# Kernel tuning notes

Measured on AMD Instinct MI355X. Metric: run time of the kernel, lower is better.

Reference implementation:

```python
import jax, jax.numpy as jnp
import numpy as np

I_SIZE, H_SIZE, O_SIZE = 3, 128, 3
B, T, A = 512, 50, 64


def _xavier(k, shape):
    fan_out, fan_in = shape
    limit = float(np.sqrt(6.0 / (fan_in + fan_out)))
    return jax.random.uniform(k, shape, minval=-limit, maxval=limit, dtype=jnp.float32)


def setup_inputs() -> dict:
    key = jax.random.key(0)
    ks = jax.random.split(key, 6)
    src = jax.random.normal(ks[0], (B, T, A * I_SIZE), dtype=jnp.float32)
    return {
        "src": src,
        "W_ih_enc": _xavier(ks[1], (H_SIZE, I_SIZE)),
        "W_hh_enc": _xavier(ks[2], (H_SIZE, H_SIZE)),
        "b_ih_enc": jnp.zeros((H_SIZE,), jnp.float32),
        "b_hh_enc": jnp.zeros((H_SIZE,), jnp.float32),
        "W_ih_dec": _xavier(ks[3], (H_SIZE, O_SIZE)),
        "W_hh_dec": _xavier(ks[4], (H_SIZE, H_SIZE)),
        "b_ih_dec": jnp.zeros((H_SIZE,), jnp.float32),
        "b_hh_dec": jnp.zeros((H_SIZE,), jnp.float32),
        "fc_W": _xavier(ks[5], (O_SIZE, H_SIZE)),
        "fc_b": jnp.zeros((O_SIZE,), jnp.float32),
        "pred_len": 12,
    }


def reference(src, W_ih_enc, W_hh_enc, b_ih_enc, b_hh_enc,
              W_ih_dec, W_hh_dec, b_ih_dec, b_hh_dec, fc_W, fc_b, pred_len):
    b, t, f = src.shape
    a = f // I_SIZE
    # (b, t, a*I) -> (t, b*a, I): agents batched together (vectorizes the per-agent loop)
    xs = src.reshape(b, t, a, I_SIZE).transpose(1, 0, 2, 3).reshape(t, b * a, I_SIZE)

    def enc_step(h, x_t):
        h = jnp.tanh(x_t @ W_ih_enc.T + b_ih_enc + h @ W_hh_enc.T + b_hh_enc)
        return h, None

    h0 = jnp.zeros((b * a, H_SIZE), src.dtype)
    h_enc, _ = jax.lax.scan(enc_step, h0, xs)

    # decoder input = last observed position of each agent
    dec_in0 = xs[-1]  # (b*a, I)

    def dec_step(carry, _):
        h, inp = carry
        h = jnp.tanh(inp @ W_ih_dec.T + b_ih_dec + h @ W_hh_dec.T + b_hh_dec)
        pred = h @ fc_W.T + fc_b  # (b*a, O)
        return (h, pred), pred

    _, preds = jax.lax.scan(dec_step, (h_enc, dec_in0), None, length=pred_len)
    # (pred_len, b*a, O) -> (b, pred_len, a*O)
    out = preds.reshape(pred_len, b, a, O_SIZE).transpose(1, 0, 2, 3).reshape(b, pred_len, a * O_SIZE)
    return out
```

## Files before the change

### kernel.cpp

```cpp
#include <hip/hip_runtime.h>
#include <stdint.h>

typedef _Float16 f16x8 __attribute__((ext_vector_type(8)));
typedef float f32x4 __attribute__((ext_vector_type(4)));
typedef unsigned int u32x4 __attribute__((ext_vector_type(4)));

#define NT 8
#define NKT 5
#define T_OBS 50
#define PRED 12

#define DEC_OFF 20480
#define FC_OFF  40960
#define WS_ELEMS 43008

__device__ __forceinline__ int unperm(int k) {
  return (k & 3) | (((k >> 3) & 3) << 2) | (((k >> 2) & 1) << 4) | (k & 0x60);
}

__global__ void prep_kernel(const float* __restrict__ Wih_e, const float* __restrict__ Whh_e,
                            const float* __restrict__ bih_e, const float* __restrict__ bhh_e,
                            const float* __restrict__ Wih_d, const float* __restrict__ Whh_d,
                            const float* __restrict__ bih_d, const float* __restrict__ bhh_d,
                            const float* __restrict__ fcW,
                            unsigned short* __restrict__ ws) {
  int idx = blockIdx.x * 256 + threadIdx.x;
  if (idx >= WS_ELEMS) return;
  float val = 0.0f;
  if (idx < FC_OFF) {
    const bool enc = idx < DEC_OFF;
    const int e = enc ? idx : idx - DEC_OFF;
    const int j = e & 7;
    const int lane = (e >> 3) & 63;
    const int rem = e >> 9;
    const int kt = rem % 5;
    const int t = rem / 5;
    const int n = 16 * t + (lane & 15);
    const int kappa = 32 * kt + ((lane >> 4) << 3) + j;
    const float* Wih = enc ? Wih_e : Wih_d;
    const float* Whh = enc ? Whh_e : Whh_d;
    const float* bih = enc ? bih_e : bih_d;
    const float* bhh = enc ? bhh_e : bhh_d;
    if (kappa < 128)       val = Whh[n * 128 + unperm(kappa)];
    else if (kappa < 131)  val = Wih[n * 3 + (kappa - 128)];
    else if (kappa == 131) val = bih[n] + bhh[n];
  } else {
    const int e = idx - FC_OFF;
    const int j = e & 7;
    const int lane = (e >> 3) & 63;
    const int kt = e >> 9;
    const int o = lane & 15;
    const int kappa = 32 * kt + ((lane >> 4) << 3) + j;
    if (o < 3) val = fcW[o * 128 + unperm(kappa)];
  }
  _Float16 h = (_Float16)val;
  ws[idx] = __builtin_bit_cast(unsigned short, h);
}

__device__ __forceinline__ float tanh_fast(float v) {
  float e = __builtin_amdgcn_exp2f(v * 2.8853900817779268f);
  return 1.0f - 2.0f * __builtin_amdgcn_rcpf(1.0f + e);
}

__global__ __launch_bounds__(256, 2) void traj_kernel(
    const float* __restrict__ src, const unsigned short* __restrict__ ws,
    const float* __restrict__ fcb, float* __restrict__ out) {
  const int lane = (int)(threadIdx.x & 63u);
  const int wave = (int)(threadIdx.x >> 6u);
  const int seq = blockIdx.x * 64 + wave * 16 + (lane & 15);
  const int b = seq >> 6;
  const int a = seq & 63;
  const bool act = (lane >> 4) == 0;

  f16x8 A[NT * NKT];
  #pragma unroll
  for (int i = 0; i < NT * NKT; ++i) {
    u32x4 raw = *(const u32x4*)(ws + (size_t)(i * 64 + lane) * 8);
    A[i] = __builtin_bit_cast(f16x8, raw);
  }

  const float* xp = src + (size_t)b * (T_OBS * 192) + a * 3;
  float x0 = xp[0], x1 = xp[1], x2 = xp[2];

  f16x8 Bf[4];
  #pragma unroll
  for (int kt = 0; kt < 4; ++kt) {
    #pragma unroll
    for (int i = 0; i < 8; ++i) Bf[kt][i] = (_Float16)0.0f;
  }
  f16x8 xf;
  #pragma unroll
  for (int i = 0; i < 8; ++i) xf[i] = (_Float16)0.0f;
  if (act) { xf[0] = (_Float16)x0; xf[1] = (_Float16)x1; xf[2] = (_Float16)x2; xf[3] = (_Float16)1.0f; }

  for (int s = 0; s < T_OBS; ++s) {
    const int t2 = (s < T_OBS - 1) ? s + 1 : s;
    const float nx0 = xp[t2 * 192 + 0];
    const float nx1 = xp[t2 * 192 + 1];
    const float nx2 = xp[t2 * 192 + 2];

    f32x4 acc[NT];
    #pragma unroll
    for (int t = 0; t < NT; ++t) acc[t] = (f32x4){0.f, 0.f, 0.f, 0.f};

    #pragma unroll
    for (int kt = 0; kt < 4; ++kt) {
      #pragma unroll
      for (int t = 0; t < NT; ++t)
        acc[t] = __builtin_amdgcn_mfma_f32_16x16x32_f16(A[t * NKT + kt], Bf[kt], acc[t], 0, 0, 0);
    }
    #pragma unroll
    for (int t = 0; t < NT; ++t)
      acc[t] = __builtin_amdgcn_mfma_f32_16x16x32_f16(A[t * NKT + 4], xf, acc[t], 0, 0, 0);

    #pragma unroll
    for (int kt = 0; kt < 4; ++kt) {
      #pragma unroll
      for (int q = 0; q < 4; ++q) {
        Bf[kt][q]     = (_Float16)tanh_fast(acc[2 * kt][q]);
        Bf[kt][4 + q] = (_Float16)tanh_fast(acc[2 * kt + 1][q]);
      }
    }
    x0 = nx0; x1 = nx1; x2 = nx2;
    #pragma unroll
    for (int i = 0; i < 8; ++i) xf[i] = (_Float16)0.0f;
    if (act) { xf[0] = (_Float16)x0; xf[1] = (_Float16)x1; xf[2] = (_Float16)x2; xf[3] = (_Float16)1.0f; }
  }

  #pragma unroll
  for (int i = 0; i < NT * NKT; ++i) {
    u32x4 raw = *(const u32x4*)(ws + DEC_OFF + (size_t)(i * 64 + lane) * 8);
    A[i] = __builtin_bit_cast(f16x8, raw);
  }
  f16x8 Afc[4];
  #pragma unroll
  for (int kt = 0; kt < 4; ++kt) {
    u32x4 raw = *(const u32x4*)(ws + FC_OFF + (size_t)(kt * 64 + lane) * 8);
    Afc[kt] = __builtin_bit_cast(f16x8, raw);
  }
  const float fb0 = fcb[0], fb1 = fcb[1], fb2 = fcb[2];

  float* op = out + (size_t)b * (PRED * 192) + a * 3;

  for (int p = 0; p < PRED; ++p) {
    f32x4 acc[NT];
    #pragma unroll
    for (int t = 0; t < NT; ++t) acc[t] = (f32x4){0.f, 0.f, 0.f, 0.f};

    #pragma unroll
    for (int kt = 0; kt < 4; ++kt) {
      #pragma unroll
      for (int t = 0; t < NT; ++t)
        acc[t] = __builtin_amdgcn_mfma_f32_16x16x32_f16(A[t * NKT + kt], Bf[kt], acc[t], 0, 0, 0);
    }
    #pragma unroll
    for (int t = 0; t < NT; ++t)
      acc[t] = __builtin_amdgcn_mfma_f32_16x16x32_f16(A[t * NKT + 4], xf, acc[t], 0, 0, 0);

    #pragma unroll
    for (int kt = 0; kt < 4; ++kt) {
      #pragma unroll
      for (int q = 0; q < 4; ++q) {
        Bf[kt][q]     = (_Float16)tanh_fast(acc[2 * kt][q]);
        Bf[kt][4 + q] = (_Float16)tanh_fast(acc[2 * kt + 1][q]);
      }
    }

    f32x4 pf = (f32x4){0.f, 0.f, 0.f, 0.f};
    #pragma unroll
    for (int kt = 0; kt < 4; ++kt)
      pf = __builtin_amdgcn_mfma_f32_16x16x32_f16(Afc[kt], Bf[kt], pf, 0, 0, 0);

    const float p0 = pf[0] + fb0;
    const float p1 = pf[1] + fb1;
    const float p2 = pf[2] + fb2;
    if (act) {
      op[p * 192 + 0] = p0;
      op[p * 192 + 1] = p1;
      op[p * 192 + 2] = p2;
    }
    #pragma unroll
    for (int i = 0; i < 8; ++i) xf[i] = (_Float16)0.0f;
    if (act) { xf[0] = (_Float16)p0; xf[1] = (_Float16)p1; xf[2] = (_Float16)p2; xf[3] = (_Float16)1.0f; }
  }
}

extern "C" void kernel_launch(void* const* d_in, const int* in_sizes, int n_in,
                              void* d_out, int out_size, void* d_ws, size_t ws_size,
                              hipStream_t stream) {
  const float* src   = (const float*)d_in[0];
  const float* Wih_e = (const float*)d_in[1];
  const float* Whh_e = (const float*)d_in[2];
  const float* bih_e = (const float*)d_in[3];
  const float* bhh_e = (const float*)d_in[4];
  const float* Wih_d = (const float*)d_in[5];
  const float* Whh_d = (const float*)d_in[6];
  const float* bih_d = (const float*)d_in[7];
  const float* bhh_d = (const float*)d_in[8];
  const float* fcW   = (const float*)d_in[9];
  const float* fcb   = (const float*)d_in[10];
  (void)in_sizes; (void)n_in; (void)out_size; (void)ws_size;

  unsigned short* ws = (unsigned short*)d_ws;

  prep_kernel<<<(WS_ELEMS + 255) / 256, 256, 0, stream>>>(
      Wih_e, Whh_e, bih_e, bhh_e, Wih_d, Whh_d, bih_d, bhh_d, fcW, ws);

  traj_kernel<<<512, 256, 0, stream>>>(src, ws, fcb, (float*)d_out);
}
```

Measured before the change: 98.46 us.

## Split hidden units across four waves with LDS exchange per timestep

Each block now handles 16 sequences, with each of the 4 waves computing 32 of the 128 hidden units. New hidden states are exchanged through a double-buffered shared-memory array with a block barrier each step. The grid grows from 512 to 2048 blocks. This shortens the per-wave dependent MFMA chain and cuts register pressure so more waves can hide latency, at the cost of per-step barriers, LDS traffic, and duplicated fc work.

```diff
diff --git a/kernel.cpp b/kernel.cpp
--- a/kernel.cpp
+++ b/kernel.cpp
@@ -62,21 +62,26 @@
   return 1.0f - 2.0f * __builtin_amdgcn_rcpf(1.0f + e);
 }
 
-__global__ __launch_bounds__(256, 2) void traj_kernel(
+__global__ __launch_bounds__(256, 4) void traj_kernel(
     const float* __restrict__ src, const unsigned short* __restrict__ ws,
     const float* __restrict__ fcb, float* __restrict__ out) {
+  __shared__ unsigned short xch[2][4][64][8];
+
   const int lane = (int)(threadIdx.x & 63u);
-  const int wave = (int)(threadIdx.x >> 6u);
-  const int seq = blockIdx.x * 64 + wave * 16 + (lane & 15);
+  const int w = (int)(threadIdx.x >> 6u);
+  const int seq = blockIdx.x * 16 + (lane & 15);
   const int b = seq >> 6;
   const int a = seq & 63;
   const bool act = (lane >> 4) == 0;
 
-  f16x8 A[NT * NKT];
-  #pragma unroll
-  for (int i = 0; i < NT * NKT; ++i) {
-    u32x4 raw = *(const u32x4*)(ws + (size_t)(i * 64 + lane) * 8);
-    A[i] = __builtin_bit_cast(f16x8, raw);
+  f16x8 A[2 * NKT];
+  #pragma unroll
+  for (int i = 0; i < 2; ++i) {
+    #pragma unroll
+    for (int kt = 0; kt < NKT; ++kt) {
+      u32x4 raw = *(const u32x4*)(ws + (size_t)((((2 * w + i) * NKT) + kt) * 64 + lane) * 8);
+      A[i * NKT + kt] = __builtin_bit_cast(f16x8, raw);
+    }
   }
 
   const float* xp = src + (size_t)b * (T_OBS * 192) + a * 3;
@@ -84,10 +89,10 @@
 
   f16x8 Bf[4];
   #pragma unroll
-  for (int kt = 0; kt < 4; ++kt) {
+  for (int kt = 0; kt < 4; ++kt)
     #pragma unroll
     for (int i = 0; i < 8; ++i) Bf[kt][i] = (_Float16)0.0f;
-  }
+
   f16x8 xf;
   #pragma unroll
   for (int i = 0; i < 8; ++i) xf[i] = (_Float16)0.0f;
@@ -99,28 +104,28 @@
     const float nx1 = xp[t2 * 192 + 1];
     const float nx2 = xp[t2 * 192 + 2];
 
-    f32x4 acc[NT];
-    #pragma unroll
-    for (int t = 0; t < NT; ++t) acc[t] = (f32x4){0.f, 0.f, 0.f, 0.f};
-
+    f32x4 acc0 = (f32x4){0.f, 0.f, 0.f, 0.f};
+    f32x4 acc1 = (f32x4){0.f, 0.f, 0.f, 0.f};
     #pragma unroll
     for (int kt = 0; kt < 4; ++kt) {
-      #pragma unroll
-      for (int t = 0; t < NT; ++t)
-        acc[t] = __builtin_amdgcn_mfma_f32_16x16x32_f16(A[t * NKT + kt], Bf[kt], acc[t], 0, 0, 0);
-    }
-    #pragma unroll
-    for (int t = 0; t < NT; ++t)
-      acc[t] = __builtin_amdgcn_mfma_f32_16x16x32_f16(A[t * NKT + 4], xf, acc[t], 0, 0, 0);
-
-    #pragma unroll
-    for (int kt = 0; kt < 4; ++kt) {
-      #pragma unroll
-      for (int q = 0; q < 4; ++q) {
-        Bf[kt][q]     = (_Float16)tanh_fast(acc[2 * kt][q]);
-        Bf[kt][4 + q] = (_Float16)tanh_fast(acc[2 * kt + 1][q]);
-      }
-    }
+      acc0 = __builtin_amdgcn_mfma_f32_16x16x32_f16(A[kt],       Bf[kt], acc0, 0, 0, 0);
+      acc1 = __builtin_amdgcn_mfma_f32_16x16x32_f16(A[NKT + kt], Bf[kt], acc1, 0, 0, 0);
+    }
+    acc0 = __builtin_amdgcn_mfma_f32_16x16x32_f16(A[4],       xf, acc0, 0, 0, 0);
+    acc1 = __builtin_amdgcn_mfma_f32_16x16x32_f16(A[NKT + 4], xf, acc1, 0, 0, 0);
+
+    f16x8 nb;
+    #pragma unroll
+    for (int q = 0; q < 4; ++q) {
+      nb[q]     = (_Float16)tanh_fast(acc0[q]);
+      nb[4 + q] = (_Float16)tanh_fast(acc1[q]);
+    }
+    *(u32x4*)&xch[s & 1][w][lane][0] = __builtin_bit_cast(u32x4, nb);
+    __syncthreads();
+    #pragma unroll
+    for (int kt = 0; kt < 4; ++kt)
+      Bf[kt] = __builtin_bit_cast(f16x8, *(const u32x4*)&xch[s & 1][kt][lane][0]);
+
     x0 = nx0; x1 = nx1; x2 = nx2;
     #pragma unroll
     for (int i = 0; i < 8; ++i) xf[i] = (_Float16)0.0f;
@@ -128,9 +133,12 @@
   }
 
   #pragma unroll
-  for (int i = 0; i < NT * NKT; ++i) {
-    u32x4 raw = *(const u32x4*)(ws + DEC_OFF + (size_t)(i * 64 + lane) * 8);
-    A[i] = __builtin_bit_cast(f16x8, raw);
+  for (int i = 0; i < 2; ++i) {
+    #pragma unroll
+    for (int kt = 0; kt < NKT; ++kt) {
+      u32x4 raw = *(const u32x4*)(ws + DEC_OFF + (size_t)((((2 * w + i) * NKT) + kt) * 64 + lane) * 8);
+      A[i * NKT + kt] = __builtin_bit_cast(f16x8, raw);
+    }
   }
   f16x8 Afc[4];
   #pragma unroll
@@ -143,28 +151,27 @@
   float* op = out + (size_t)b * (PRED * 192) + a * 3;
 
   for (int p = 0; p < PRED; ++p) {
-    f32x4 acc[NT];
-    #pragma unroll
-    for (int t = 0; t < NT; ++t) acc[t] = (f32x4){0.f, 0.f, 0.f, 0.f};
-
+    f32x4 acc0 = (f32x4){0.f, 0.f, 0.f, 0.f};
+    f32x4 acc1 = (f32x4){0.f, 0.f, 0.f, 0.f};
     #pragma unroll
     for (int kt = 0; kt < 4; ++kt) {
-      #pragma unroll
-      for (int t = 0; t < NT; ++t)
-        acc[t] = __builtin_amdgcn_mfma_f32_16x16x32_f16(A[t * NKT + kt], Bf[kt], acc[t], 0, 0, 0);
-    }
-    #pragma unroll
-    for (int t = 0; t < NT; ++t)
-      acc[t] = __builtin_amdgcn_mfma_f32_16x16x32_f16(A[t * NKT + 4], xf, acc[t], 0, 0, 0);
-
-    #pragma unroll
-    for (int kt = 0; kt < 4; ++kt) {
-      #pragma unroll
-      for (int q = 0; q < 4; ++q) {
-        Bf[kt][q]     = (_Float16)tanh_fast(acc[2 * kt][q]);
-        Bf[kt][4 + q] = (_Float16)tanh_fast(acc[2 * kt + 1][q]);
-      }
-    }
+      acc0 = __builtin_amdgcn_mfma_f32_16x16x32_f16(A[kt],       Bf[kt], acc0, 0, 0, 0);
+      acc1 = __builtin_amdgcn_mfma_f32_16x16x32_f16(A[NKT + kt], Bf[kt], acc1, 0, 0, 0);
+    }
+    acc0 = __builtin_amdgcn_mfma_f32_16x16x32_f16(A[4],       xf, acc0, 0, 0, 0);
+    acc1 = __builtin_amdgcn_mfma_f32_16x16x32_f16(A[NKT + 4], xf, acc1, 0, 0, 0);
+
+    f16x8 nb;
+    #pragma unroll
+    for (int q = 0; q < 4; ++q) {
+      nb[q]     = (_Float16)tanh_fast(acc0[q]);
+      nb[4 + q] = (_Float16)tanh_fast(acc1[q]);
+    }
+    *(u32x4*)&xch[p & 1][w][lane][0] = __builtin_bit_cast(u32x4, nb);
+    __syncthreads();
+    #pragma unroll
+    for (int kt = 0; kt < 4; ++kt)
+      Bf[kt] = __builtin_bit_cast(f16x8, *(const u32x4*)&xch[p & 1][kt][lane][0]);
 
     f32x4 pf = (f32x4){0.f, 0.f, 0.f, 0.f};
     #pragma unroll
@@ -174,7 +181,7 @@
     const float p0 = pf[0] + fb0;
     const float p1 = pf[1] + fb1;
     const float p2 = pf[2] + fb2;
-    if (act) {
+    if (w == 0 && act) {
       op[p * 192 + 0] = p0;
       op[p * 192 + 1] = p1;
       op[p * 192 + 2] = p2;
@@ -206,5 +213,5 @@
   prep_kernel<<<(WS_ELEMS + 255) / 256, 256, 0, stream>>>(
       Wih_e, Whh_e, bih_e, bhh_e, Wih_d, Whh_d, bih_d, bhh_d, fcW, ws);
 
-  traj_kernel<<<512, 256, 0, stream>>>(src, ws, fcb, (float*)d_out);
-}
+  traj_kernel<<<2048, 256, 0, stream>>>(src, ws, fcb, (float*)d_out);
+}
```

Measured after the change: 102.8 us. 4.4% more time.

## Switch RNN to 32x32x16 MFMA with two waves splitting hidden units via LDS

Applied to the files above, without the earlier changes.

The recurrence now uses 32x32x16 MFMAs over 32 sequences per block, replacing 16x16x32 tiles that wasted three quarters of the B columns on inactive lanes. Two waves each compute half of the 128 hidden units and swap their tanh outputs through double-buffered shared memory with a barrier every step. The change also packs f16 conversions with cvt_pkrtz and fuses the tanh tail into an FMA. It adds a per-step __syncthreads and LDS traffic on the serial critical path, and launches twice as many smaller blocks.

```diff
diff --git a/kernel.cpp b/kernel.cpp
--- a/kernel.cpp
+++ b/kernel.cpp
@@ -2,20 +2,19 @@
 #include <stdint.h>
 
 typedef _Float16 f16x8 __attribute__((ext_vector_type(8)));
-typedef float f32x4 __attribute__((ext_vector_type(4)));
+typedef _Float16 f16x2 __attribute__((ext_vector_type(2)));
+typedef float f32x16 __attribute__((ext_vector_type(16)));
 typedef unsigned int u32x4 __attribute__((ext_vector_type(4)));
 
-#define NT 8
-#define NKT 5
 #define T_OBS 50
 #define PRED 12
 
-#define DEC_OFF 20480
-#define FC_OFF  40960
-#define WS_ELEMS 43008
-
-__device__ __forceinline__ int unperm(int k) {
-  return (k & 3) | (((k >> 3) & 3) << 2) | (((k >> 2) & 1) << 4) | (k & 0x60);
+#define DEC_OFF 18432
+#define FC_OFF  36864
+#define WS_ELEMS 40960
+
+__device__ __forceinline__ int swap23(int k) {
+  return (k & ~12) | ((k & 4) << 1) | ((k & 8) >> 1);
 }
 
 __global__ void prep_kernel(const float* __restrict__ Wih_e, const float* __restrict__ Whh_e,
@@ -27,31 +26,34 @@
   int idx = blockIdx.x * 256 + threadIdx.x;
   if (idx >= WS_ELEMS) return;
   float val = 0.0f;
+  const int j = idx & 7;
+  const int lane = (idx >> 3) & 63;
+  const int hi = lane >> 5;
+  const int mlo = lane & 31;
   if (idx < FC_OFF) {
     const bool enc = idx < DEC_OFF;
     const int e = enc ? idx : idx - DEC_OFF;
-    const int j = e & 7;
-    const int lane = (e >> 3) & 63;
     const int rem = e >> 9;
-    const int kt = rem % 5;
-    const int t = rem / 5;
-    const int n = 16 * t + (lane & 15);
-    const int kappa = 32 * kt + ((lane >> 4) << 3) + j;
+    const int kt = rem % 9;
+    const int T = rem / 9;
+    const int m = 32 * T + mlo;
     const float* Wih = enc ? Wih_e : Wih_d;
     const float* Whh = enc ? Whh_e : Whh_d;
     const float* bih = enc ? bih_e : bih_d;
     const float* bhh = enc ? bhh_e : bhh_d;
-    if (kappa < 128)       val = Whh[n * 128 + unperm(kappa)];
-    else if (kappa < 131)  val = Wih[n * 3 + (kappa - 128)];
-    else if (kappa == 131) val = bih[n] + bhh[n];
+    if (kt < 8) {
+      const int kap = 16 * kt + 8 * hi + j;
+      val = Whh[m * 128 + swap23(kap)];
+    } else {
+      const int c = 8 * hi + j;
+      if (c < 3) val = Wih[m * 3 + c];
+      else if (c == 3) val = bih[m] + bhh[m];
+    }
   } else {
     const int e = idx - FC_OFF;
-    const int j = e & 7;
-    const int lane = (e >> 3) & 63;
     const int kt = e >> 9;
-    const int o = lane & 15;
-    const int kappa = 32 * kt + ((lane >> 4) << 3) + j;
-    if (o < 3) val = fcW[o * 128 + unperm(kappa)];
+    const int kap = 16 * kt + 8 * hi + j;
+    if (mlo < 3) val = fcW[mlo * 128 + swap23(kap)];
   }
   _Float16 h = (_Float16)val;
   ws[idx] = __builtin_bit_cast(unsigned short, h);
@@ -59,129 +61,133 @@
 
 __device__ __forceinline__ float tanh_fast(float v) {
   float e = __builtin_amdgcn_exp2f(v * 2.8853900817779268f);
-  return 1.0f - 2.0f * __builtin_amdgcn_rcpf(1.0f + e);
-}
-
-__global__ __launch_bounds__(256, 2) void traj_kernel(
+  return __builtin_fmaf(-2.0f, __builtin_amdgcn_rcpf(1.0f + e), 1.0f);
+}
+
+__device__ __forceinline__ unsigned int pk2(float a, float b) {
+  return __builtin_bit_cast(unsigned int, __builtin_amdgcn_cvt_pkrtz(a, b));
+}
+
+__device__ __forceinline__ f16x8 ldfrag(const unsigned short* p) {
+  return __builtin_bit_cast(f16x8, *(const u32x4*)p);
+}
+
+__global__ __launch_bounds__(128, 2) void traj_kernel(
     const float* __restrict__ src, const unsigned short* __restrict__ ws,
     const float* __restrict__ fcb, float* __restrict__ out) {
+  __shared__ unsigned short xch[2][2][4][64][8];
+
   const int lane = (int)(threadIdx.x & 63u);
-  const int wave = (int)(threadIdx.x >> 6u);
-  const int seq = blockIdx.x * 64 + wave * 16 + (lane & 15);
+  const int w = (int)(threadIdx.x >> 6u);
+  const int seq = blockIdx.x * 32 + (lane & 31);
   const int b = seq >> 6;
   const int a = seq & 63;
-  const bool act = (lane >> 4) == 0;
-
-  f16x8 A[NT * NKT];
-  #pragma unroll
-  for (int i = 0; i < NT * NKT; ++i) {
-    u32x4 raw = *(const u32x4*)(ws + (size_t)(i * 64 + lane) * 8);
-    A[i] = __builtin_bit_cast(f16x8, raw);
-  }
-
-  const float* xp = src + (size_t)b * (T_OBS * 192) + a * 3;
-  float x0 = xp[0], x1 = xp[1], x2 = xp[2];
-
-  f16x8 Bf[4];
-  #pragma unroll
-  for (int kt = 0; kt < 4; ++kt) {
-    #pragma unroll
-    for (int i = 0; i < 8; ++i) Bf[kt][i] = (_Float16)0.0f;
-  }
-  f16x8 xf;
-  #pragma unroll
-  for (int i = 0; i < 8; ++i) xf[i] = (_Float16)0.0f;
-  if (act) { xf[0] = (_Float16)x0; xf[1] = (_Float16)x1; xf[2] = (_Float16)x2; xf[3] = (_Float16)1.0f; }
-
-  for (int s = 0; s < T_OBS; ++s) {
-    const int t2 = (s < T_OBS - 1) ? s + 1 : s;
-    const float nx0 = xp[t2 * 192 + 0];
-    const float nx1 = xp[t2 * 192 + 1];
-    const float nx2 = xp[t2 * 192 + 2];
-
-    f32x4 acc[NT];
-    #pragma unroll
-    for (int t = 0; t < NT; ++t) acc[t] = (f32x4){0.f, 0.f, 0.f, 0.f};
-
-    #pragma unroll
-    for (int kt = 0; kt < 4; ++kt) {
-      #pragma unroll
-      for (int t = 0; t < NT; ++t)
-        acc[t] = __builtin_amdgcn_mfma_f32_16x16x32_f16(A[t * NKT + kt], Bf[kt], acc[t], 0, 0, 0);
-    }
-    #pragma unroll
-    for (int t = 0; t < NT; ++t)
-      acc[t] = __builtin_amdgcn_mfma_f32_16x16x32_f16(A[t * NKT + 4], xf, acc[t], 0, 0, 0);
-
-    #pragma unroll
-    for (int kt = 0; kt < 4; ++kt) {
-      #pragma unroll
-      for (int q = 0; q < 4; ++q) {
-        Bf[kt][q]     = (_Float16)tanh_fast(acc[2 * kt][q]);
-        Bf[kt][4 + q] = (_Float16)tanh_fast(acc[2 * kt + 1][q]);
-      }
-    }
-    x0 = nx0; x1 = nx1; x2 = nx2;
-    #pragma unroll
-    for (int i = 0; i < 8; ++i) xf[i] = (_Float16)0.0f;
-    if (act) { xf[0] = (_Float16)x0; xf[1] = (_Float16)x1; xf[2] = (_Float16)x2; xf[3] = (_Float16)1.0f; }
-  }
-
-  #pragma unroll
-  for (int i = 0; i < NT * NKT; ++i) {
-    u32x4 raw = *(const u32x4*)(ws + DEC_OFF + (size_t)(i * 64 + lane) * 8);
-    A[i] = __builtin_bit_cast(f16x8, raw);
-  }
-  f16x8 Afc[4];
-  #pragma unroll
-  for (int kt = 0; kt < 4; ++kt) {
-    u32x4 raw = *(const u32x4*)(ws + FC_OFF + (size_t)(kt * 64 + lane) * 8);
-    Afc[kt] = __builtin_bit_cast(f16x8, raw);
-  }
+
+  f16x8 A[2][9];
+  #pragma unroll
+  for (int t = 0; t < 2; ++t)
+    #pragma unroll
+    for (int kt = 0; kt < 9; ++kt)
+      A[t][kt] = ldfrag(ws + (size_t)(((2 * w + t) * 9 + kt) * 64 + lane) * 8);
+
+  const float* xq = src + (size_t)b * (T_OBS * 192) + a * 3;
+  float x0 = xq[0], x1 = xq[1], x2 = xq[2];
+  xq += 192;
+
+  f16x8 Bf[8];
+  #pragma unroll
+  for (int kt = 0; kt < 8; ++kt) {
+    u32x4 zz = (u32x4)0u;
+    Bf[kt] = __builtin_bit_cast(f16x8, zz);
+  }
+
+  u32x4 xfu = (u32x4)0u;
+  xfu[0] = pk2(x0, x1);
+  xfu[1] = pk2(x2, 1.0f);
+
+  const f32x16 z = (f32x16)0.0f;
+
+  auto rnn_step = [&](int par) {
+    f16x8 xf = __builtin_bit_cast(f16x8, xfu);
+    f32x16 a0 = __builtin_amdgcn_mfma_f32_32x32x16_f16(A[0][8], xf, z, 0, 0, 0);
+    f32x16 a1 = __builtin_amdgcn_mfma_f32_32x32x16_f16(A[1][8], xf, z, 0, 0, 0);
+    #pragma unroll
+    for (int kt = 0; kt < 8; ++kt) {
+      a0 = __builtin_amdgcn_mfma_f32_32x32x16_f16(A[0][kt], Bf[kt], a0, 0, 0, 0);
+      a1 = __builtin_amdgcn_mfma_f32_32x32x16_f16(A[1][kt], Bf[kt], a1, 0, 0, 0);
+    }
+    u32x4 F0, F1, F2, F3;
+    #pragma unroll
+    for (int q = 0; q < 4; ++q) {
+      F0[q] = pk2(tanh_fast(a0[2 * q]),     tanh_fast(a0[2 * q + 1]));
+      F1[q] = pk2(tanh_fast(a0[8 + 2 * q]), tanh_fast(a0[8 + 2 * q + 1]));
+      F2[q] = pk2(tanh_fast(a1[2 * q]),     tanh_fast(a1[2 * q + 1]));
+      F3[q] = pk2(tanh_fast(a1[8 + 2 * q]), tanh_fast(a1[8 + 2 * q + 1]));
+    }
+    *(u32x4*)&xch[par][w][0][lane][0] = F0;
+    *(u32x4*)&xch[par][w][1][lane][0] = F1;
+    *(u32x4*)&xch[par][w][2][lane][0] = F2;
+    *(u32x4*)&xch[par][w][3][lane][0] = F3;
+    __syncthreads();
+    if (w == 0) {
+      Bf[0] = __builtin_bit_cast(f16x8, F0);
+      Bf[1] = __builtin_bit_cast(f16x8, F1);
+      Bf[2] = __builtin_bit_cast(f16x8, F2);
+      Bf[3] = __builtin_bit_cast(f16x8, F3);
+      Bf[4] = ldfrag(&xch[par][1][0][lane][0]);
+      Bf[5] = ldfrag(&xch[par][1][1][lane][0]);
+      Bf[6] = ldfrag(&xch[par][1][2][lane][0]);
+      Bf[7] = ldfrag(&xch[par][1][3][lane][0]);
+    } else {
+      Bf[4] = __builtin_bit_cast(f16x8, F0);
+      Bf[5] = __builtin_bit_cast(f16x8, F1);
+      Bf[6] = __builtin_bit_cast(f16x8, F2);
+      Bf[7] = __builtin_bit_cast(f16x8, F3);
+      Bf[0] = ldfrag(&xch[par][0][0][lane][0]);
+      Bf[1] = ldfrag(&xch[par][0][1][lane][0]);
+      Bf[2] = ldfrag(&xch[par][0][2][lane][0]);
+      Bf[3] = ldfrag(&xch[par][0][3][lane][0]);
+    }
+  };
+
+  for (int s = 0; s < T_OBS - 1; ++s) {
+    const float nx0 = xq[0], nx1 = xq[1], nx2 = xq[2];
+    xq += 192;
+    rnn_step(s & 1);
+    xfu[0] = pk2(nx0, nx1);
+    xfu[1] = pk2(nx2, 1.0f);
+  }
+  rnn_step(1);
+
+  #pragma unroll
+  for (int t = 0; t < 2; ++t)
+    #pragma unroll
+    for (int kt = 0; kt < 9; ++kt)
+      A[t][kt] = ldfrag(ws + DEC_OFF + (size_t)(((2 * w + t) * 9 + kt) * 64 + lane) * 8);
+  f16x8 Afc[8];
+  #pragma unroll
+  for (int kt = 0; kt < 8; ++kt)
+    Afc[kt] = ldfrag(ws + FC_OFF + (size_t)(kt * 64 + lane) * 8);
   const float fb0 = fcb[0], fb1 = fcb[1], fb2 = fcb[2];
 
   float* op = out + (size_t)b * (PRED * 192) + a * 3;
 
   for (int p = 0; p < PRED; ++p) {
-    f32x4 acc[NT];
-    #pragma unroll
-    for (int t = 0; t < NT; ++t) acc[t] = (f32x4){0.f, 0.f, 0.f, 0.f};
-
-    #pragma unroll
-    for (int kt = 0; kt < 4; ++kt) {
-      #pragma unroll
-      for (int t = 0; t < NT; ++t)
-        acc[t] = __builtin_amdgcn_mfma_f32_16x16x32_f16(A[t * NKT + kt], Bf[kt], acc[t], 0, 0, 0);
-    }
-    #pragma unroll
-    for (int t = 0; t < NT; ++t)
-      acc[t] = __builtin_amdgcn_mfma_f32_16x16x32_f16(A[t * NKT + 4], xf, acc[t], 0, 0, 0);
-
-    #pragma unroll
-    for (int kt = 0; kt < 4; ++kt) {
-      #pragma unroll
-      for (int q = 0; q < 4; ++q) {
-        Bf[kt][q]     = (_Float16)tanh_fast(acc[2 * kt][q]);
-        Bf[kt][4 + q] = (_Float16)tanh_fast(acc[2 * kt + 1][q]);
-      }
-    }
-
-    f32x4 pf = (f32x4){0.f, 0.f, 0.f, 0.f};
-    #pragma unroll
-    for (int kt = 0; kt < 4; ++kt)
-      pf = __builtin_amdgcn_mfma_f32_16x16x32_f16(Afc[kt], Bf[kt], pf, 0, 0, 0);
-
+    rnn_step(p & 1);
+    f32x16 pf = __builtin_amdgcn_mfma_f32_32x32x16_f16(Afc[0], Bf[0], z, 0, 0, 0);
+    #pragma unroll
+    for (int kt = 1; kt < 8; ++kt)
+      pf = __builtin_amdgcn_mfma_f32_32x32x16_f16(Afc[kt], Bf[kt], pf, 0, 0, 0);
     const float p0 = pf[0] + fb0;
     const float p1 = pf[1] + fb1;
     const float p2 = pf[2] + fb2;
-    if (act) {
+    if (w == 0 && lane < 32) {
       op[p * 192 + 0] = p0;
       op[p * 192 + 1] = p1;
       op[p * 192 + 2] = p2;
     }
-    #pragma unroll
-    for (int i = 0; i < 8; ++i) xf[i] = (_Float16)0.0f;
-    if (act) { xf[0] = (_Float16)p0; xf[1] = (_Float16)p1; xf[2] = (_Float16)p2; xf[3] = (_Float16)1.0f; }
+    xfu[0] = pk2(p0, p1);
+    xfu[1] = pk2(p2, 1.0f);
   }
 }
 
@@ -206,5 +212,5 @@
   prep_kernel<<<(WS_ELEMS + 255) / 256, 256, 0, stream>>>(
       Wih_e, Whh_e, bih_e, bhh_e, Wih_d, Whh_d, bih_d, bhh_d, fcW, ws);
 
-  traj_kernel<<<512, 256, 0, stream>>>(src, ws, fcb, (float*)d_out);
-}
+  traj_kernel<<<1024, 128, 0, stream>>>(src, ws, fcb, (float*)d_out);
+}
```

Measured after the change: 205.8 us. 109% more time.

## Split hidden dimension across waves with LDS exchange of recurrent state

Applied to the files above, without the earlier changes.

Each block now handles 32 sequences, and each of its four waves computes a 32-row slice of the hidden state for two 16-sequence groups, instead of one wave computing all 128 rows for 16 sequences. The new hidden-state slices are exchanged through double-buffered shared memory with a block barrier every step. The k-tile order is rotated per wave so the locally produced fragment is reused directly. The goal is to cut the serial MFMA chain per wave, lower register pressure (launch bounds go to 3 blocks per SIMD) and double the grid, at the cost of a __syncthreads and LDS traffic on every recurrent step. Packed fp16 conversion via cvt_pkrtz is also used.

```diff
diff --git a/kernel.cpp b/kernel.cpp
--- a/kernel.cpp
+++ b/kernel.cpp
@@ -5,8 +5,6 @@
 typedef float f32x4 __attribute__((ext_vector_type(4)));
 typedef unsigned int u32x4 __attribute__((ext_vector_type(4)));
 
-#define NT 8
-#define NKT 5
 #define T_OBS 50
 #define PRED 12
 
@@ -59,129 +57,136 @@
 
 __device__ __forceinline__ float tanh_fast(float v) {
   float e = __builtin_amdgcn_exp2f(v * 2.8853900817779268f);
-  return 1.0f - 2.0f * __builtin_amdgcn_rcpf(1.0f + e);
-}
-
-__global__ __launch_bounds__(256, 2) void traj_kernel(
+  return __builtin_fmaf(-2.0f, __builtin_amdgcn_rcpf(1.0f + e), 1.0f);
+}
+
+__device__ __forceinline__ unsigned int pk2(float a, float b) {
+  return __builtin_bit_cast(unsigned int, __builtin_amdgcn_cvt_pkrtz(a, b));
+}
+
+__device__ __forceinline__ f16x8 ldfrag(const unsigned short* p) {
+  return __builtin_bit_cast(f16x8, *(const u32x4*)p);
+}
+
+__device__ __forceinline__ f16x8 mkxf(float a, float b, float c) {
+  u32x4 u;
+  u[0] = pk2(a, b);
+  u[1] = pk2(c, 1.0f);
+  u[2] = 0u;
+  u[3] = 0u;
+  return __builtin_bit_cast(f16x8, u);
+}
+
+__global__ __launch_bounds__(256, 3) void traj_kernel(
     const float* __restrict__ src, const unsigned short* __restrict__ ws,
     const float* __restrict__ fcb, float* __restrict__ out) {
+  __shared__ unsigned short xch[2][4][2][64][8];
+
   const int lane = (int)(threadIdx.x & 63u);
-  const int wave = (int)(threadIdx.x >> 6u);
-  const int seq = blockIdx.x * 64 + wave * 16 + (lane & 15);
-  const int b = seq >> 6;
-  const int a = seq & 63;
-  const bool act = (lane >> 4) == 0;
-
-  f16x8 A[NT * NKT];
-  #pragma unroll
-  for (int i = 0; i < NT * NKT; ++i) {
-    u32x4 raw = *(const u32x4*)(ws + (size_t)(i * 64 + lane) * 8);
-    A[i] = __builtin_bit_cast(f16x8, raw);
-  }
-
-  const float* xp = src + (size_t)b * (T_OBS * 192) + a * 3;
-  float x0 = xp[0], x1 = xp[1], x2 = xp[2];
-
-  f16x8 Bf[4];
-  #pragma unroll
-  for (int kt = 0; kt < 4; ++kt) {
+  const int w = (int)(threadIdx.x >> 6u);
+  const int l15 = lane & 15;
+  const int sA = blockIdx.x * 32 + l15;
+  const int sB = sA + 16;
+  const float* xpA = src + (size_t)(sA >> 6) * (T_OBS * 192) + (sA & 63) * 3;
+  const float* xpB = src + (size_t)(sB >> 6) * (T_OBS * 192) + (sB & 63) * 3;
+
+  f16x8 A0[5], A1[5];
+  #pragma unroll
+  for (int i = 0; i < 5; ++i) {
+    const int kt = (i < 4) ? ((w + i) & 3) : 4;
+    A0[i] = ldfrag(ws + (size_t)(((2 * w)     * 5 + kt) * 64 + lane) * 8);
+    A1[i] = ldfrag(ws + (size_t)(((2 * w + 1) * 5 + kt) * 64 + lane) * 8);
+  }
+
+  f16x8 B0[4], B1[4];
+  #pragma unroll
+  for (int i = 0; i < 4; ++i) {
+    u32x4 zz = (u32x4)0u;
+    B0[i] = __builtin_bit_cast(f16x8, zz);
+    B1[i] = __builtin_bit_cast(f16x8, zz);
+  }
+
+  f16x8 xf0 = mkxf(xpA[0], xpA[1], xpA[2]);
+  f16x8 xf1 = mkxf(xpB[0], xpB[1], xpB[2]);
+
+  auto rnn_step = [&](int par, f16x8 xfa, f16x8 xfb) {
+    const f32x4 z = (f32x4){0.f, 0.f, 0.f, 0.f};
+    f32x4 aA = __builtin_amdgcn_mfma_f32_16x16x32_f16(A0[4], xfa, z, 0, 0, 0);
+    f32x4 aB = __builtin_amdgcn_mfma_f32_16x16x32_f16(A1[4], xfa, z, 0, 0, 0);
+    f32x4 aC = __builtin_amdgcn_mfma_f32_16x16x32_f16(A0[4], xfb, z, 0, 0, 0);
+    f32x4 aD = __builtin_amdgcn_mfma_f32_16x16x32_f16(A1[4], xfb, z, 0, 0, 0);
     #pragma unroll
-    for (int i = 0; i < 8; ++i) Bf[kt][i] = (_Float16)0.0f;
-  }
-  f16x8 xf;
-  #pragma unroll
-  for (int i = 0; i < 8; ++i) xf[i] = (_Float16)0.0f;
-  if (act) { xf[0] = (_Float16)x0; xf[1] = (_Float16)x1; xf[2] = (_Float16)x2; xf[3] = (_Float16)1.0f; }
+    for (int i = 0; i < 4; ++i) {
+      aA = __builtin_amdgcn_mfma_f32_16x16x32_f16(A0[i], B0[i], aA, 0, 0, 0);
+      aB = __builtin_amdgcn_mfma_f32_16x16x32_f16(A1[i], B0[i], aB, 0, 0, 0);
+      aC = __builtin_amdgcn_mfma_f32_16x16x32_f16(A0[i], B1[i], aC, 0, 0, 0);
+      aD = __builtin_amdgcn_mfma_f32_16x16x32_f16(A1[i], B1[i], aD, 0, 0, 0);
+    }
+    u32x4 F0, F1;
+    F0[0] = pk2(tanh_fast(aA[0]), tanh_fast(aA[1]));
+    F0[1] = pk2(tanh_fast(aA[2]), tanh_fast(aA[3]));
+    F0[2] = pk2(tanh_fast(aB[0]), tanh_fast(aB[1]));
+    F0[3] = pk2(tanh_fast(aB[2]), tanh_fast(aB[3]));
+    F1[0] = pk2(tanh_fast(aC[0]), tanh_fast(aC[1]));
+    F1[1] = pk2(tanh_fast(aC[2]), tanh_fast(aC[3]));
+    F1[2] = pk2(tanh_fast(aD[0]), tanh_fast(aD[1]));
+    F1[3] = pk2(tanh_fast(aD[2]), tanh_fast(aD[3]));
+    *(u32x4*)&xch[par][w][0][lane][0] = F0;
+    *(u32x4*)&xch[par][w][1][lane][0] = F1;
+    __syncthreads();
+    B0[0] = __builtin_bit_cast(f16x8, F0);
+    B1[0] = __builtin_bit_cast(f16x8, F1);
+    #pragma unroll
+    for (int i = 1; i < 4; ++i) {
+      B0[i] = ldfrag(&xch[par][(w + i) & 3][0][lane][0]);
+      B1[i] = ldfrag(&xch[par][(w + i) & 3][1][lane][0]);
+    }
+  };
 
   for (int s = 0; s < T_OBS; ++s) {
     const int t2 = (s < T_OBS - 1) ? s + 1 : s;
-    const float nx0 = xp[t2 * 192 + 0];
-    const float nx1 = xp[t2 * 192 + 1];
-    const float nx2 = xp[t2 * 192 + 2];
-
-    f32x4 acc[NT];
+    const float na0 = xpA[t2 * 192], na1 = xpA[t2 * 192 + 1], na2 = xpA[t2 * 192 + 2];
+    const float nb0 = xpB[t2 * 192], nb1 = xpB[t2 * 192 + 1], nb2 = xpB[t2 * 192 + 2];
+    rnn_step(s & 1, xf0, xf1);
+    xf0 = mkxf(na0, na1, na2);
+    xf1 = mkxf(nb0, nb1, nb2);
+  }
+
+  #pragma unroll
+  for (int i = 0; i < 5; ++i) {
+    const int kt = (i < 4) ? ((w + i) & 3) : 4;
+    A0[i] = ldfrag(ws + DEC_OFF + (size_t)(((2 * w)     * 5 + kt) * 64 + lane) * 8);
+    A1[i] = ldfrag(ws + DEC_OFF + (size_t)(((2 * w + 1) * 5 + kt) * 64 + lane) * 8);
+  }
+  f16x8 Afc[4];
+  #pragma unroll
+  for (int i = 0; i < 4; ++i) {
+    const int kt = (w + i) & 3;
+    Afc[i] = ldfrag(ws + FC_OFF + (size_t)(kt * 64 + lane) * 8);
+  }
+  const float fb0 = fcb[0], fb1 = fcb[1], fb2 = fcb[2];
+
+  float* opA = out + (size_t)(sA >> 6) * (PRED * 192) + (sA & 63) * 3;
+  float* opB = out + (size_t)(sB >> 6) * (PRED * 192) + (sB & 63) * 3;
+
+  for (int p = 0; p < PRED; ++p) {
+    rnn_step(p & 1, xf0, xf1);
+    const f32x4 z = (f32x4){0.f, 0.f, 0.f, 0.f};
+    f32x4 pA = __builtin_amdgcn_mfma_f32_16x16x32_f16(Afc[0], B0[0], z, 0, 0, 0);
+    f32x4 pB = __builtin_amdgcn_mfma_f32_16x16x32_f16(Afc[0], B1[0], z, 0, 0, 0);
     #pragma unroll
-    for (int t = 0; t < NT; ++t) acc[t] = (f32x4){0.f, 0.f, 0.f, 0.f};
-
-    #pragma unroll
-    for (int kt = 0; kt < 4; ++kt) {
-      #pragma unroll
-      for (int t = 0; t < NT; ++t)
-        acc[t] = __builtin_amdgcn_mfma_f32_16x16x32_f16(A[t * NKT + kt], Bf[kt], acc[t], 0, 0, 0);
-    }
-    #pragma unroll
-    for (int t = 0; t < NT; ++t)
-      acc[t] = __builtin_amdgcn_mfma_f32_16x16x32_f16(A[t * NKT + 4], xf, acc[t], 0, 0, 0);
-
-    #pragma unroll
-    for (int kt = 0; kt < 4; ++kt) {
-      #pragma unroll
-      for (int q = 0; q < 4; ++q) {
-        Bf[kt][q]     = (_Float16)tanh_fast(acc[2 * kt][q]);
-        Bf[kt][4 + q] = (_Float16)tanh_fast(acc[2 * kt + 1][q]);
-      }
-    }
-    x0 = nx0; x1 = nx1; x2 = nx2;
-    #pragma unroll
-    for (int i = 0; i < 8; ++i) xf[i] = (_Float16)0.0f;
-    if (act) { xf[0] = (_Float16)x0; xf[1] = (_Float16)x1; xf[2] = (_Float16)x2; xf[3] = (_Float16)1.0f; }
-  }
-
-  #pragma unroll
-  for (int i = 0; i < NT * NKT; ++i) {
-    u32x4 raw = *(const u32x4*)(ws + DEC_OFF + (size_t)(i * 64 + lane) * 8);
-    A[i] = __builtin_bit_cast(f16x8, raw);
-  }
-  f16x8 Afc[4];
-  #pragma unroll
-  for (int kt = 0; kt < 4; ++kt) {
-    u32x4 raw = *(const u32x4*)(ws + FC_OFF + (size_t)(kt * 64 + lane) * 8);
-    Afc[kt] = __builtin_bit_cast(f16x8, raw);
-  }
-  const float fb0 = fcb[0], fb1 = fcb[1], fb2 = fcb[2];
-
-  float* op = out + (size_t)b * (PRED * 192) + a * 3;
-
-  for (int p = 0; p < PRED; ++p) {
-    f32x4 acc[NT];
-    #pragma unroll
-    for (int t = 0; t < NT; ++t) acc[t] = (f32x4){0.f, 0.f, 0.f, 0.f};
-
-    #pragma unroll
-    for (int kt = 0; kt < 4; ++kt) {
-      #pragma unroll
-      for (int t = 0; t < NT; ++t)
-        acc[t] = __builtin_amdgcn_mfma_f32_16x16x32_f16(A[t * NKT + kt], Bf[kt], acc[t], 0, 0, 0);
-    }
-    #pragma unroll
-    for (int t = 0; t < NT; ++t)
-      acc[t] = __builtin_amdgcn_mfma_f32_16x16x32_f16(A[t * NKT + 4], xf, acc[t], 0, 0, 0);
-
-    #pragma unroll
-    for (int kt = 0; kt < 4; ++kt) {
-      #pragma unroll
-      for (int q = 0; q < 4; ++q) {
-        Bf[kt][q]     = (_Float16)tanh_fast(acc[2 * kt][q]);
-        Bf[kt][4 + q] = (_Float16)tanh_fast(acc[2 * kt + 1][q]);
-      }
-    }
-
-    f32x4 pf = (f32x4){0.f, 0.f, 0.f, 0.f};
-    #pragma unroll
-    for (int kt = 0; kt < 4; ++kt)
-      pf = __builtin_amdgcn_mfma_f32_16x16x32_f16(Afc[kt], Bf[kt], pf, 0, 0, 0);
-
-    const float p0 = pf[0] + fb0;
-    const float p1 = pf[1] + fb1;
-    const float p2 = pf[2] + fb2;
-    if (act) {
-      op[p * 192 + 0] = p0;
-      op[p * 192 + 1] = p1;
-      op[p * 192 + 2] = p2;
-    }
-    #pragma unroll
-    for (int i = 0; i < 8; ++i) xf[i] = (_Float16)0.0f;
-    if (act) { xf[0] = (_Float16)p0; xf[1] = (_Float16)p1; xf[2] = (_Float16)p2; xf[3] = (_Float16)1.0f; }
+    for (int i = 1; i < 4; ++i) {
+      pA = __builtin_amdgcn_mfma_f32_16x16x32_f16(Afc[i], B0[i], pA, 0, 0, 0);
+      pB = __builtin_amdgcn_mfma_f32_16x16x32_f16(Afc[i], B1[i], pB, 0, 0, 0);
+    }
+    const float pa0 = pA[0] + fb0, pa1 = pA[1] + fb1, pa2 = pA[2] + fb2;
+    const float pb0 = pB[0] + fb0, pb1 = pB[1] + fb1, pb2 = pB[2] + fb2;
+    if (w == 0 && lane < 16) {
+      opA[p * 192 + 0] = pa0; opA[p * 192 + 1] = pa1; opA[p * 192 + 2] = pa2;
+      opB[p * 192 + 0] = pb0; opB[p * 192 + 1] = pb1; opB[p * 192 + 2] = pb2;
+    }
+    xf0 = mkxf(pa0, pa1, pa2);
+    xf1 = mkxf(pb0, pb1, pb2);
   }
 }
 
@@ -206,5 +211,5 @@
   prep_kernel<<<(WS_ELEMS + 255) / 256, 256, 0, stream>>>(
       Wih_e, Whh_e, bih_e, bhh_e, Wih_d, Whh_d, bih_d, bhh_d, fcW, ws);
 
-  traj_kernel<<<512, 256, 0, stream>>>(src, ws, fcb, (float*)d_out);
-}
+  traj_kernel<<<1024, 256, 0, stream>>>(src, ws, fcb, (float*)d_out);
+}
```

Measured after the change: 99.02 us. About the same (+0.6%).
